# Optimization experiments

Hardware: AMD Instinct MI355X
Metric: run time of the kernel (lower is better)

## Reference

```python
import jax, jax.numpy as jnp
import numpy as np

N_NODES = 100000
N_EDGES = 1600000
IN_C, HID_C, OUT_C = 64, 64, 32


def setup_inputs() -> dict:
    key = jax.random.key(0)
    ks = jax.random.split(key, 6)
    x = jax.random.normal(ks[0], (N_NODES, IN_C), dtype=jnp.float32)
    edge_index = jax.random.randint(ks[1], (2, N_EDGES), 0, N_NODES, dtype=jnp.int64)
    edge_weight = jax.random.uniform(ks[2], (N_EDGES,), dtype=jnp.float32)
    # Glorot-ish init for the two GCNConv weight matrices, zero bias (PyG default)
    W1 = jax.random.normal(ks[3], (IN_C, HID_C), dtype=jnp.float32) / np.sqrt(IN_C)
    b1 = jnp.zeros((HID_C,), dtype=jnp.float32)
    W2 = jax.random.normal(ks[4], (HID_C, OUT_C), dtype=jnp.float32) / np.sqrt(HID_C)
    b2 = jnp.zeros((OUT_C,), dtype=jnp.float32)
    return {"x": x, "edge_index": edge_index, "edge_weight": edge_weight,
            "W1": W1, "b1": b1, "W2": W2, "b2": b2}


def _gcn_conv(x, src, dst, w, W, b):
    """PyG GCNConv: add self-loops (weight 1), symmetric D^-1/2 (A+I) D^-1/2 norm,
    then aggregate transformed features into destination nodes, plus bias."""
    n = x.shape[0]
    loop = jnp.arange(n, dtype=src.dtype)
    s = jnp.concatenate([src, loop])
    d = jnp.concatenate([dst, loop])
    wl = jnp.concatenate([w, jnp.ones((n,), dtype=x.dtype)])
    deg = jax.ops.segment_sum(wl, d, num_segments=n)            # [N]
    dinv = jnp.where(deg > 0, jax.lax.rsqrt(deg), 0.0)
    norm = dinv[s] * wl * dinv[d]                               # [E+N]
    xw = x @ W                                                  # [N, C_out]
    msg = norm[:, None] * xw[s]                                 # gather + scale
    return jax.ops.segment_sum(msg, d, num_segments=n) + b      # scatter-add


def reference(x, edge_index, edge_weight, W1, b1, W2, b2):
    src, dst = edge_index[0], edge_index[1]
    h = _gcn_conv(x, src, dst, edge_weight, W1, b1)
    h = jax.nn.relu(h)
    # dropout(p=0.5, training=self.training): identity in eval mode
    return _gcn_conv(h, src, dst, edge_weight, W2, b2)
```

## Files before the change

kernel.cpp:

```cpp
#include <hip/hip_runtime.h>

#define N_NODES 100000
#define N_EDGES 1600000
#define IN_C 64
#define HID_C 64
#define OUT_C 32

#define NB 391
#define BSHIFT 8
#define BMASK 255
#define SEG_CAP 4864
#define EPB 4096
#define BIN_BLOCKS ((N_EDGES + EPB - 1) / EPB)
#define G1_BLOCKS ((N_NODES + 63) / 64)
#define SMASK 0x1FFFF
#define FIXSCALE 34359738368.0f

__device__ __forceinline__ unsigned int bpack(float a, float b) {
    unsigned int ua = __float_as_uint(a);
    ua += 0x7FFFu + ((ua >> 16) & 1u);
    unsigned int ub = __float_as_uint(b);
    ub += 0x7FFFu + ((ub >> 16) & 1u);
    return (ua >> 16) | (ub & 0xFFFF0000u);
}
__device__ __forceinline__ float2 bup(unsigned int v) {
    return make_float2(__uint_as_float(v << 16), __uint_as_float(v & 0xFFFF0000u));
}


struct BinSh {
    int2 recs[EPB];
    int meta[EPB];
    int hist[NB];
    int gbase[NB];
};
struct G1Sh {
    float XsT[64][64];
    float Ws[64][64];
};
union FusedSh { BinSh b; G1Sh g; };

__global__ void __launch_bounds__(256) fused1_kernel(
    const int* __restrict__ src, const int* __restrict__ dst,
    const float* __restrict__ w, int* __restrict__ gcnt, int2* __restrict__ seg,
    const float* __restrict__ X, const float* __restrict__ W,
    unsigned int* __restrict__ XWu) {
    __shared__ FusedSh sh;
    int tid = threadIdx.x;
    if (blockIdx.x < BIN_BLOCKS) {
        for (int i = tid; i < NB; i += 256) sh.b.hist[i] = 0;
        __syncthreads();
        int e0 = blockIdx.x * EPB;
        int n = min(EPB, N_EDGES - e0);
        const int4* src4 = (const int4*)(src + e0);
        const int4* dst4 = (const int4*)(dst + e0);
        const float4* w4 = (const float4*)(w + e0);
        int n4 = n >> 2;
        for (int i = tid; i < n4; i += 256) {
            int4 s = src4[i];
            int4 d = dst4[i];
            float4 ww = w4[i];
#define BIN_ONE(K, SS, DD, WW)                                             \
            {                                                              \
                int b = (DD) >> BSHIFT;                                    \
                int slot = K * n4 + i;                                     \
                sh.b.recs[slot] = make_int2((SS) | (((DD) & BMASK) << 17), \
                                            __float_as_int(WW));           \
                int rank = atomicAdd(&sh.b.hist[b], 1);                    \
                sh.b.meta[slot] = b | (rank << 9);                         \
            }
            BIN_ONE(0, s.x, d.x, ww.x)
            BIN_ONE(1, s.y, d.y, ww.y)
            BIN_ONE(2, s.z, d.z, ww.z)
            BIN_ONE(3, s.w, d.w, ww.w)
#undef BIN_ONE
        }
        __syncthreads();
        for (int b = tid; b < NB; b += 256) {
            int c = sh.b.hist[b];
            sh.b.gbase[b] = c ? atomicAdd(&gcnt[b], c) : 0;
        }
        __syncthreads();
        for (int i = tid; i < n; i += 256) {
            int m = sh.b.meta[i];
            int b = m & 511, rank = m >> 9;
            int pos = sh.b.gbase[b] + rank;
            if (pos < SEG_CAP) seg[(size_t)b * SEG_CAP + pos] = sh.b.recs[i];
        }
    } else {
        {
            const float4* Wv = (const float4*)W;
            float4* Wsv = (float4*)&sh.g.Ws[0][0];
            for (int i = tid; i < 1024; i += 256) Wsv[i] = Wv[i];
        }
        int row0 = (blockIdx.x - BIN_BLOCKS) * 64;
        int rmax = N_NODES - row0;
        for (int i = tid; i < 64 * 16; i += 256) {
            int r = i & 63, kq = i >> 6;
            float4 v = (r < rmax) ? ((const float4*)(X + (size_t)(row0 + r) * IN_C))[kq]
                                  : make_float4(0.f, 0.f, 0.f, 0.f);
            sh.g.XsT[4 * kq + 0][r] = v.x;
            sh.g.XsT[4 * kq + 1][r] = v.y;
            sh.g.XsT[4 * kq + 2][r] = v.z;
            sh.g.XsT[4 * kq + 3][r] = v.w;
        }
        __syncthreads();
        int tr = tid >> 4, tc = tid & 15;
        float acc[4][4] = {};
        float a[4], bb[4];
#pragma unroll 8
        for (int k = 0; k < 64; ++k) {
            *(float4*)a = *(const float4*)&sh.g.XsT[k][4 * tr];
            *(float4*)bb = *(const float4*)&sh.g.Ws[k][4 * tc];
#pragma unroll
            for (int i = 0; i < 4; ++i)
#pragma unroll
                for (int j = 0; j < 4; ++j) acc[i][j] += a[i] * bb[j];
        }
#pragma unroll
        for (int i = 0; i < 4; ++i) {
            int rl = 4 * tr + i;
            if (rl < rmax) {
                int row = row0 + rl;
                uint2 o;
                o.x = bpack(acc[i][0], acc[i][1]);
                o.y = bpack(acc[i][2], acc[i][3]);
                ((uint2*)XWu)[(size_t)row * 16 + tc] = o;
            }
        }
    }
}


__global__ void __launch_bounds__(256) bsort_kernel(const int* __restrict__ gcnt,
                                                    const int2* __restrict__ seg,
                                                    int2* __restrict__ seg2,
                                                    float* __restrict__ dinv,
                                                    int2* __restrict__ rowRC,
                                                    unsigned int* __restrict__ XWs) {
    __shared__ int2 recs[SEG_CAP];
    __shared__ unsigned long long packed[256];
    __shared__ int meta[SEG_CAP];
    __shared__ int sarr[256];
    __shared__ int ofs0[256];
    __shared__ float dinvsh[256];
    int tid = threadIdx.x, b = blockIdx.x;
    int n = min(gcnt[b], SEG_CAP);
    const int2* sp = seg + (size_t)b * SEG_CAP;
    packed[tid] = 0ULL;
    __syncthreads();
    for (int i = tid; i < n; i += 256) {
        int2 r = sp[i];
        recs[i] = r;
        int dl = (r.x >> 17) & BMASK;
        unsigned long long fixw =
            (unsigned long long)(__int_as_float(r.y) * FIXSCALE);
        unsigned long long old = atomicAdd(&packed[dl], (1ULL << 48) | fixw);
        meta[i] = dl | ((int)(old >> 48) << 8);
    }
    __syncthreads();
    unsigned long long p = packed[tid];
    int myc = (int)(p >> 48);
    float degw = (float)((double)(p & ((1ULL << 48) - 1)) * (1.0 / (double)FIXSCALE));
    float dv = rsqrtf(1.0f + degw);
    dinvsh[tid] = dv;
    int node = (b << BSHIFT) + tid;
    if (node < N_NODES) dinv[node] = dv;
    int padc = (myc + 1) & ~1;
    sarr[tid] = padc;
    __syncthreads();
    for (int off = 1; off < 256; off <<= 1) {
        int tmp = (tid >= off) ? sarr[tid - off] : 0;
        __syncthreads();
        sarr[tid] += tmp;
        __syncthreads();
    }
    int excl = sarr[tid] - padc;
    if (node < N_NODES) rowRC[node] = make_int2(b * SEG_CAP + excl, myc);
    ofs0[tid] = excl;
    __syncthreads();
    int2* op = seg2 + (size_t)b * SEG_CAP;
    for (int i = tid; i < n; i += 256) {
        int m = meta[i];
        int dl = m & BMASK, rank = m >> 8;
        op[ofs0[dl] + rank] = recs[i];
    }
    int baseRow = b << BSHIFT;
    int rowsHere = min(256, N_NODES - baseRow);
    uint4* XW4 = (uint4*)XWs;
    for (int i = tid; i < rowsHere * 8; i += 256) {
        int nl = i >> 3;
        float s = dinvsh[nl];
        uint4 v = XW4[(size_t)(baseRow + nl) * 8 + (i & 7)];
        float2 f;
        f = bup(v.x); v.x = bpack(f.x * s, f.y * s);
        f = bup(v.y); v.y = bpack(f.x * s, f.y * s);
        f = bup(v.z); v.z = bpack(f.x * s, f.y * s);
        f = bup(v.w); v.w = bpack(f.x * s, f.y * s);
        XW4[(size_t)(baseRow + nl) * 8 + (i & 7)] = v;
    }
}


__global__ void __launch_bounds__(256) agg1_kernel(const int2* __restrict__ rowRC,
                                                   const int2* __restrict__ seg2,
                                                   const unsigned int* __restrict__ XWs,
                                                   const float* __restrict__ dinv,
                                                   const float* __restrict__ b1,
                                                   unsigned int* __restrict__ Hb) {
    int l16 = threadIdx.x & 15;
    int d = blockIdx.x * 16 + (threadIdx.x >> 4);
    if (d >= N_NODES) return;
    const uint2* XW2 = (const uint2*)XWs;
    float did = dinv[d];
    float4 bv = ((const float4*)b1)[l16];
    uint2 sv = XW2[(size_t)d * 16 + l16];
    float2 f0 = bup(sv.x), f1 = bup(sv.y);
    float a0 = bv.x + did * f0.x, a1 = bv.y + did * f0.y;
    float a2 = bv.z + did * f1.x, a3 = bv.w + did * f1.y;
    int2 rc = rowRC[d];
    int nc = rc.y;
    const int2* sp = seg2 + rc.x;
    const int4* sp4 = (const int4*)sp;
    int e = 0;
    for (; e + 8 <= nc; e += 8) {
        int4 q0 = sp4[(e >> 1) + 0], q1 = sp4[(e >> 1) + 1];
        int4 q2 = sp4[(e >> 1) + 2], q3 = sp4[(e >> 1) + 3];
        int s0 = q0.x & SMASK, s1 = q0.z & SMASK, s2 = q1.x & SMASK, s3 = q1.z & SMASK;
        int s4 = q2.x & SMASK, s5 = q2.z & SMASK, s6 = q3.x & SMASK, s7 = q3.z & SMASK;
        uint2 r0 = XW2[(size_t)s0 * 16 + l16];
        uint2 r1 = XW2[(size_t)s1 * 16 + l16];
        uint2 r2 = XW2[(size_t)s2 * 16 + l16];
        uint2 r3 = XW2[(size_t)s3 * 16 + l16];
        uint2 r4 = XW2[(size_t)s4 * 16 + l16];
        uint2 r5 = XW2[(size_t)s5 * 16 + l16];
        uint2 r6 = XW2[(size_t)s6 * 16 + l16];
        uint2 r7 = XW2[(size_t)s7 * 16 + l16];
        float c0 = __int_as_float(q0.y) * did, c1 = __int_as_float(q0.w) * did;
        float c2 = __int_as_float(q1.y) * did, c3 = __int_as_float(q1.w) * did;
        float c4 = __int_as_float(q2.y) * did, c5 = __int_as_float(q2.w) * did;
        float c6 = __int_as_float(q3.y) * did, c7 = __int_as_float(q3.w) * did;
        float2 v;
#define ACC1(R, C)                                                         \
        v = bup(R.x); a0 += (C) * v.x; a1 += (C) * v.y;                    \
        v = bup(R.y); a2 += (C) * v.x; a3 += (C) * v.y;
        ACC1(r0, c0) ACC1(r1, c1) ACC1(r2, c2) ACC1(r3, c3)
        ACC1(r4, c4) ACC1(r5, c5) ACC1(r6, c6) ACC1(r7, c7)
    }
    for (; e + 2 <= nc; e += 2) {
        int4 q = sp4[e >> 1];
        int s0 = q.x & SMASK, s1 = q.z & SMASK;
        uint2 r0 = XW2[(size_t)s0 * 16 + l16];
        uint2 r1 = XW2[(size_t)s1 * 16 + l16];
        float c0 = __int_as_float(q.y) * did, c1 = __int_as_float(q.w) * did;
        float2 v;
        ACC1(r0, c0) ACC1(r1, c1)
    }
    if (e < nc) {
        int2 p = sp[e];
        int s = p.x & SMASK;
        float c = __int_as_float(p.y) * did;
        uint2 r = XW2[(size_t)s * 16 + l16];
        float2 v;
        ACC1(r, c)
    }
#undef ACC1
    uint2 o;
    o.x = bpack(fmaxf(a0, 0.f), fmaxf(a1, 0.f));
    o.y = bpack(fmaxf(a2, 0.f), fmaxf(a3, 0.f));
    ((uint2*)Hb)[(size_t)d * 16 + l16] = o;
}


__global__ void __launch_bounds__(256) gemm2_kernel(const unsigned int* __restrict__ Hb,
                                                    const float* __restrict__ W,
                                                    const float* __restrict__ dinv,
                                                    unsigned int* __restrict__ HWs,
                                                    int nRows) {
    __shared__ float HsT[64][128];
    __shared__ float Ws[64][32];
    int tid = threadIdx.x;
    {
        const float4* Wv = (const float4*)W;
        float4* Wsv = (float4*)&Ws[0][0];
        for (int i = tid; i < 512; i += 256) Wsv[i] = Wv[i];
    }
    int row0 = blockIdx.x * 128;
    int rmax = nRows - row0;
    for (int i = tid; i < 128 * 8; i += 256) {
        int r = i & 127, kq = i >> 7;
        uint4 v = (r < rmax) ? ((const uint4*)(Hb + (size_t)(row0 + r) * 32))[kq]
                             : make_uint4(0u, 0u, 0u, 0u);
        float2 f;
        f = bup(v.x); HsT[8 * kq + 0][r] = f.x; HsT[8 * kq + 1][r] = f.y;
        f = bup(v.y); HsT[8 * kq + 2][r] = f.x; HsT[8 * kq + 3][r] = f.y;
        f = bup(v.z); HsT[8 * kq + 4][r] = f.x; HsT[8 * kq + 5][r] = f.y;
        f = bup(v.w); HsT[8 * kq + 6][r] = f.x; HsT[8 * kq + 7][r] = f.y;
    }
    __syncthreads();
    int tr = tid >> 3, tc = tid & 7;
    float acc[4][4] = {};
    float a[4], bb[4];
#pragma unroll 8
    for (int k = 0; k < 64; ++k) {
        *(float4*)a = *(const float4*)&HsT[k][4 * tr];
        *(float4*)bb = *(const float4*)&Ws[k][4 * tc];
#pragma unroll
        for (int i = 0; i < 4; ++i)
#pragma unroll
            for (int j = 0; j < 4; ++j) acc[i][j] += a[i] * bb[j];
    }
#pragma unroll
    for (int i = 0; i < 4; ++i) {
        int rl = 4 * tr + i;
        if (rl < rmax) {
            int row = row0 + rl;
            float di = dinv[row];
            uint2 o;
            o.x = bpack(acc[i][0] * di, acc[i][1] * di);
            o.y = bpack(acc[i][2] * di, acc[i][3] * di);
            ((uint2*)HWs)[(size_t)row * 8 + tc] = o;
        }
    }
}


__global__ void __launch_bounds__(256) agg2_kernel(const int2* __restrict__ rowRC,
                                                   const int2* __restrict__ seg2,
                                                   const unsigned int* __restrict__ HWs,
                                                   const float* __restrict__ dinv,
                                                   const float* __restrict__ b2,
                                                   float* __restrict__ out) {
    int l8 = threadIdx.x & 7;
    int d = blockIdx.x * 32 + (threadIdx.x >> 3);
    if (d >= N_NODES) return;
    const uint2* HW2 = (const uint2*)HWs;
    float did = dinv[d];
    float4 bv = ((const float4*)b2)[l8];
    uint2 sv = HW2[(size_t)d * 8 + l8];
    float2 f0 = bup(sv.x), f1 = bup(sv.y);
    float a0 = bv.x + did * f0.x, a1 = bv.y + did * f0.y;
    float a2 = bv.z + did * f1.x, a3 = bv.w + did * f1.y;
    int2 rc = rowRC[d];
    int nc = rc.y;
    const int2* sp = seg2 + rc.x;
    const int4* sp4 = (const int4*)sp;
    int e = 0;
    for (; e + 8 <= nc; e += 8) {
        int4 q0 = sp4[(e >> 1) + 0], q1 = sp4[(e >> 1) + 1];
        int4 q2 = sp4[(e >> 1) + 2], q3 = sp4[(e >> 1) + 3];
        int s0 = q0.x & SMASK, s1 = q0.z & SMASK, s2 = q1.x & SMASK, s3 = q1.z & SMASK;
        int s4 = q2.x & SMASK, s5 = q2.z & SMASK, s6 = q3.x & SMASK, s7 = q3.z & SMASK;
        uint2 r0 = HW2[(size_t)s0 * 8 + l8];
        uint2 r1 = HW2[(size_t)s1 * 8 + l8];
        uint2 r2 = HW2[(size_t)s2 * 8 + l8];
        uint2 r3 = HW2[(size_t)s3 * 8 + l8];
        uint2 r4 = HW2[(size_t)s4 * 8 + l8];
        uint2 r5 = HW2[(size_t)s5 * 8 + l8];
        uint2 r6 = HW2[(size_t)s6 * 8 + l8];
        uint2 r7 = HW2[(size_t)s7 * 8 + l8];
        float c0 = __int_as_float(q0.y) * did, c1 = __int_as_float(q0.w) * did;
        float c2 = __int_as_float(q1.y) * did, c3 = __int_as_float(q1.w) * did;
        float c4 = __int_as_float(q2.y) * did, c5 = __int_as_float(q2.w) * did;
        float c6 = __int_as_float(q3.y) * did, c7 = __int_as_float(q3.w) * did;
        float2 v;
#define ACC2(R, C)                                                         \
        v = bup(R.x); a0 += (C) * v.x; a1 += (C) * v.y;                    \
        v = bup(R.y); a2 += (C) * v.x; a3 += (C) * v.y;
        ACC2(r0, c0) ACC2(r1, c1) ACC2(r2, c2) ACC2(r3, c3)
        ACC2(r4, c4) ACC2(r5, c5) ACC2(r6, c6) ACC2(r7, c7)
    }
    for (; e + 2 <= nc; e += 2) {
        int4 q = sp4[e >> 1];
        int s0 = q.x & SMASK, s1 = q.z & SMASK;
        uint2 r0 = HW2[(size_t)s0 * 8 + l8];
        uint2 r1 = HW2[(size_t)s1 * 8 + l8];
        float c0 = __int_as_float(q.y) * did, c1 = __int_as_float(q.w) * did;
        float2 v;
        ACC2(r0, c0) ACC2(r1, c1)
    }
    if (e < nc) {
        int2 p = sp[e];
        int s = p.x & SMASK;
        float c = __int_as_float(p.y) * did;
        uint2 r = HW2[(size_t)s * 8 + l8];
        float2 v;
        ACC2(r, c)
    }
#undef ACC2
    ((float4*)out)[(size_t)d * 8 + l8] = make_float4(a0, a1, a2, a3);
}


extern "C" void kernel_launch(void* const* d_in, const int* in_sizes, int n_in,
                              void* d_out, int out_size, void* d_ws, size_t ws_size,
                              hipStream_t stream) {
    const float* x = (const float*)d_in[0];
    const int* edge_index = (const int*)d_in[1];
    const float* ew = (const float*)d_in[2];
    const float* W1 = (const float*)d_in[3];
    const float* b1 = (const float*)d_in[4];
    const float* W2 = (const float*)d_in[5];
    const float* b2 = (const float*)d_in[6];
    float* out = (float*)d_out;

    const int* src = edge_index;
    const int* dst = edge_index + N_EDGES;

    char* ws = (char*)d_ws;
    size_t off = 0;
    auto carve = [&](size_t bytes) -> void* {
        void* p = ws + off;
        off += (bytes + 255) & ~(size_t)255;
        return p;
    };

    int* gcnt = (int*)carve(NB * 4);
    float* dinv = (float*)carve((size_t)N_NODES * 4);
    int2* rowRC = (int2*)carve((size_t)N_NODES * 8);
    int2* seg = (int2*)carve((size_t)NB * SEG_CAP * 8);
    int2* seg2 = (int2*)carve((size_t)NB * SEG_CAP * 8);
    unsigned int* XWs = (unsigned int*)carve((size_t)N_NODES * 32 * 4);
    unsigned int* Hb = (unsigned int*)carve((size_t)N_NODES * 32 * 4);
    unsigned int* HWs = XWs;

    hipMemsetAsync(gcnt, 0, NB * 4, stream);
    fused1_kernel<<<BIN_BLOCKS + G1_BLOCKS, 256, 0, stream>>>(src, dst, ew, gcnt, seg,
                                                              x, W1, XWs);
    bsort_kernel<<<NB, 256, 0, stream>>>(gcnt, seg, seg2, dinv, rowRC, XWs);
    agg1_kernel<<<(N_NODES + 15) / 16, 256, 0, stream>>>(rowRC, seg2, XWs, dinv, b1, Hb);
    gemm2_kernel<<<(N_NODES + 127) / 128, 256, 0, stream>>>(Hb, W2, dinv, HWs, N_NODES);
    agg2_kernel<<<(N_NODES + 31) / 32, 256, 0, stream>>>(rowRC, seg2, HWs, dinv, b2, out);
}
```

Baseline: 222.1 us.

## Drop shared record staging in binning and sort; widen bsort blocks to 1024 threads

The binning phase now runs in two passes over the edge arrays. The first pass reads only dst to build the histogram and ranks, and the second re-reads src/dst/w and scatters records directly to global. This removes the 32KB shared int2 recs buffer, which should allow more blocks per CU. The bucket sort also stops staging records in shared memory: it re-reads them from global in the scatter pass and runs with 1024 threads per block to raise parallelism over its 391 blocks. In exchange, both kernels read their input records twice from global memory.

```diff
diff --git a/kernel.cpp b/kernel.cpp
--- a/kernel.cpp
+++ b/kernel.cpp
@@ -29,7 +29,6 @@
 
 
 struct BinSh {
-    int2 recs[EPB];
     int meta[EPB];
     int hist[NB];
     int gbase[NB];
@@ -52,40 +51,43 @@
         __syncthreads();
         int e0 = blockIdx.x * EPB;
         int n = min(EPB, N_EDGES - e0);
+        const int4* dst4 = (const int4*)(dst + e0);
+        int n4 = n >> 2;
+        for (int i = tid; i < n4; i += 256) {
+            int4 d = dst4[i];
+            int b0 = d.x >> BSHIFT, b1 = d.y >> BSHIFT;
+            int b2 = d.z >> BSHIFT, b3 = d.w >> BSHIFT;
+            sh.b.meta[0 * n4 + i] = atomicAdd(&sh.b.hist[b0], 1);
+            sh.b.meta[1 * n4 + i] = atomicAdd(&sh.b.hist[b1], 1);
+            sh.b.meta[2 * n4 + i] = atomicAdd(&sh.b.hist[b2], 1);
+            sh.b.meta[3 * n4 + i] = atomicAdd(&sh.b.hist[b3], 1);
+        }
+        __syncthreads();
+        for (int b = tid; b < NB; b += 256) {
+            int c = sh.b.hist[b];
+            sh.b.gbase[b] = c ? atomicAdd(&gcnt[b], c) : 0;
+        }
+        __syncthreads();
         const int4* src4 = (const int4*)(src + e0);
-        const int4* dst4 = (const int4*)(dst + e0);
         const float4* w4 = (const float4*)(w + e0);
-        int n4 = n >> 2;
         for (int i = tid; i < n4; i += 256) {
             int4 s = src4[i];
             int4 d = dst4[i];
             float4 ww = w4[i];
-#define BIN_ONE(K, SS, DD, WW)                                             \
+#define FL_ONE(K, SS, DD, WW)                                              \
             {                                                              \
                 int b = (DD) >> BSHIFT;                                    \
-                int slot = K * n4 + i;                                     \
-                sh.b.recs[slot] = make_int2((SS) | (((DD) & BMASK) << 17), \
-                                            __float_as_int(WW));           \
-                int rank = atomicAdd(&sh.b.hist[b], 1);                    \
-                sh.b.meta[slot] = b | (rank << 9);                         \
+                int pos = sh.b.gbase[b] + sh.b.meta[K * n4 + i];           \
+                if (pos < SEG_CAP)                                         \
+                    seg[(size_t)b * SEG_CAP + pos] =                       \
+                        make_int2((SS) | (((DD) & BMASK) << 17),           \
+                                  __float_as_int(WW));                     \
             }
-            BIN_ONE(0, s.x, d.x, ww.x)
-            BIN_ONE(1, s.y, d.y, ww.y)
-            BIN_ONE(2, s.z, d.z, ww.z)
-            BIN_ONE(3, s.w, d.w, ww.w)
-#undef BIN_ONE
-        }
-        __syncthreads();
-        for (int b = tid; b < NB; b += 256) {
-            int c = sh.b.hist[b];
-            sh.b.gbase[b] = c ? atomicAdd(&gcnt[b], c) : 0;
-        }
-        __syncthreads();
-        for (int i = tid; i < n; i += 256) {
-            int m = sh.b.meta[i];
-            int b = m & 511, rank = m >> 9;
-            int pos = sh.b.gbase[b] + rank;
-            if (pos < SEG_CAP) seg[(size_t)b * SEG_CAP + pos] = sh.b.recs[i];
+            FL_ONE(0, s.x, d.x, ww.x)
+            FL_ONE(1, s.y, d.y, ww.y)
+            FL_ONE(2, s.z, d.z, ww.z)
+            FL_ONE(3, s.w, d.w, ww.w)
+#undef FL_ONE
         }
     } else {
         {
@@ -132,13 +134,12 @@
 }
 
 
-__global__ void __launch_bounds__(256) bsort_kernel(const int* __restrict__ gcnt,
-                                                    const int2* __restrict__ seg,
-                                                    int2* __restrict__ seg2,
-                                                    float* __restrict__ dinv,
-                                                    int2* __restrict__ rowRC,
-                                                    unsigned int* __restrict__ XWs) {
-    __shared__ int2 recs[SEG_CAP];
+__global__ void __launch_bounds__(1024) bsort_kernel(const int* __restrict__ gcnt,
+                                                     const int2* __restrict__ seg,
+                                                     int2* __restrict__ seg2,
+                                                     float* __restrict__ dinv,
+                                                     int2* __restrict__ rowRC,
+                                                     unsigned int* __restrict__ XWs) {
     __shared__ unsigned long long packed[256];
     __shared__ int meta[SEG_CAP];
     __shared__ int sarr[256];
@@ -147,11 +148,10 @@
     int tid = threadIdx.x, b = blockIdx.x;
     int n = min(gcnt[b], SEG_CAP);
     const int2* sp = seg + (size_t)b * SEG_CAP;
-    packed[tid] = 0ULL;
+    if (tid < 256) packed[tid] = 0ULL;
     __syncthreads();
-    for (int i = tid; i < n; i += 256) {
+    for (int i = tid; i < n; i += 1024) {
         int2 r = sp[i];
-        recs[i] = r;
         int dl = (r.x >> 17) & BMASK;
         unsigned long long fixw =
             (unsigned long long)(__int_as_float(r.y) * FIXSCALE);
@@ -159,36 +159,44 @@
         meta[i] = dl | ((int)(old >> 48) << 8);
     }
     __syncthreads();
-    unsigned long long p = packed[tid];
-    int myc = (int)(p >> 48);
-    float degw = (float)((double)(p & ((1ULL << 48) - 1)) * (1.0 / (double)FIXSCALE));
-    float dv = rsqrtf(1.0f + degw);
-    dinvsh[tid] = dv;
-    int node = (b << BSHIFT) + tid;
-    if (node < N_NODES) dinv[node] = dv;
-    int padc = (myc + 1) & ~1;
-    sarr[tid] = padc;
+    int myc = 0, padc = 0;
+    if (tid < 256) {
+        unsigned long long p = packed[tid];
+        myc = (int)(p >> 48);
+        float degw = (float)((double)(p & ((1ULL << 48) - 1)) * (1.0 / (double)FIXSCALE));
+        float dv = rsqrtf(1.0f + degw);
+        dinvsh[tid] = dv;
+        int node = (b << BSHIFT) + tid;
+        if (node < N_NODES) dinv[node] = dv;
+        padc = (myc + 1) & ~1;
+        sarr[tid] = padc;
+    }
     __syncthreads();
     for (int off = 1; off < 256; off <<= 1) {
-        int tmp = (tid >= off) ? sarr[tid - off] : 0;
-        __syncthreads();
-        sarr[tid] += tmp;
-        __syncthreads();
-    }
-    int excl = sarr[tid] - padc;
-    if (node < N_NODES) rowRC[node] = make_int2(b * SEG_CAP + excl, myc);
-    ofs0[tid] = excl;
+        int tmp = 0;
+        if (tid < 256 && tid >= off) tmp = sarr[tid - off];
+        __syncthreads();
+        if (tid < 256) sarr[tid] += tmp;
+        __syncthreads();
+    }
+    if (tid < 256) {
+        int excl = sarr[tid] - padc;
+        int node = (b << BSHIFT) + tid;
+        if (node < N_NODES) rowRC[node] = make_int2(b * SEG_CAP + excl, myc);
+        ofs0[tid] = excl;
+    }
     __syncthreads();
     int2* op = seg2 + (size_t)b * SEG_CAP;
-    for (int i = tid; i < n; i += 256) {
+    for (int i = tid; i < n; i += 1024) {
+        int2 r = sp[i];
         int m = meta[i];
         int dl = m & BMASK, rank = m >> 8;
-        op[ofs0[dl] + rank] = recs[i];
+        op[ofs0[dl] + rank] = r;
     }
     int baseRow = b << BSHIFT;
     int rowsHere = min(256, N_NODES - baseRow);
     uint4* XW4 = (uint4*)XWs;
-    for (int i = tid; i < rowsHere * 8; i += 256) {
+    for (int i = tid; i < rowsHere * 8; i += 1024) {
         int nl = i >> 3;
         float s = dinvsh[nl];
         uint4 v = XW4[(size_t)(baseRow + nl) * 8 + (i & 7)];
@@ -427,7 +435,7 @@
     hipMemsetAsync(gcnt, 0, NB * 4, stream);
     fused1_kernel<<<BIN_BLOCKS + G1_BLOCKS, 256, 0, stream>>>(src, dst, ew, gcnt, seg,
                                                               x, W1, XWs);
-    bsort_kernel<<<NB, 256, 0, stream>>>(gcnt, seg, seg2, dinv, rowRC, XWs);
+    bsort_kernel<<<NB, 1024, 0, stream>>>(gcnt, seg, seg2, dinv, rowRC, XWs);
     agg1_kernel<<<(N_NODES + 15) / 16, 256, 0, stream>>>(rowRC, seg2, XWs, dinv, b1, Hb);
     gemm2_kernel<<<(N_NODES + 127) / 128, 256, 0, stream>>>(Hb, W2, dinv, HWs, N_NODES);
     agg2_kernel<<<(N_NODES + 31) / 32, 256, 0, stream>>>(rowRC, seg2, HWs, dinv, b2, out);
```

Result: faster. 217.0 us (-2.3%).
